# Optimization experiments

Measured on AMD Instinct MI355X. Metric: run time of the kernel, lower is better.

The kernel has to match this reference:

```python
import jax, jax.numpy as jnp
import numpy as np

NUM_GRIDS = 8
GRID = jnp.linspace(-2.0, 2.0, NUM_GRIDS)
DENOM = 4.0 / (NUM_GRIDS - 1)
H, D = 8, 64
Q_DIM = K_DIM = V_DIM = 512
TOT = H * D


def fastkan(x, ln_s, ln_b, sw, bw, bb):
    # LayerNorm over last dim
    mu = jnp.mean(x, axis=-1, keepdims=True)
    var = jnp.var(x, axis=-1, keepdims=True)
    xn = (x - mu) * jax.lax.rsqrt(var + 1e-5) * ln_s + ln_b
    # Gaussian RBF basis over fixed grid: [..., in, G]
    basis = jnp.exp(-jnp.square((xn[..., None] - GRID) / DENOM))
    flat = basis.reshape(*x.shape[:-1], x.shape[-1] * NUM_GRIDS)
    # spline linear + base update (silu -> linear)
    return flat @ sw.T + jax.nn.silu(x) @ bw.T + bb


def setup_inputs() -> dict:
    key = jax.random.key(0)
    keys = iter(jax.random.split(key, 32))
    B, QL, KL = 2, 2048, 2048
    inp = {
        "q": jax.random.normal(next(keys), (B, QL, Q_DIM), jnp.float32),
        "k": jax.random.normal(next(keys), (B, KL, K_DIM), jnp.float32),
        "v": jax.random.normal(next(keys), (B, KL, V_DIM), jnp.float32),
    }
    def layer(ind, outd):
        return {
            "ln_s": jnp.ones((ind,), jnp.float32),
            "ln_b": jnp.zeros((ind,), jnp.float32),
            "sw": jax.random.normal(next(keys), (outd, ind * NUM_GRIDS), jnp.float32) * (0.1 / np.sqrt(ind * NUM_GRIDS)),
            "bw": jax.random.normal(next(keys), (outd, ind), jnp.float32) / np.sqrt(ind),
            "bb": jnp.zeros((outd,), jnp.float32),
        }
    dims = {"lq": (Q_DIM, TOT), "lk": (K_DIM, TOT), "lv": (V_DIM, TOT), "lo": (TOT, Q_DIM), "lg": (Q_DIM, TOT)}
    for name, (i, o) in dims.items():
        for pn, arr in layer(i, o).items():
            inp[name + "_" + pn] = arr
    return inp


def reference(q, k, v,
              lq_ln_s, lq_ln_b, lq_sw, lq_bw, lq_bb,
              lk_ln_s, lk_ln_b, lk_sw, lk_bw, lk_bb,
              lv_ln_s, lv_ln_b, lv_sw, lv_bw, lv_bb,
              lo_ln_s, lo_ln_b, lo_sw, lo_bw, lo_bb,
              lg_ln_s, lg_ln_b, lg_sw, lg_bw, lg_bb):
    norm = D ** -0.5
    wq = fastkan(q, lq_ln_s, lq_ln_b, lq_sw, lq_bw, lq_bb).reshape(*q.shape[:-1], H, D) * norm
    wk = fastkan(k, lk_ln_s, lk_ln_b, lk_sw, lk_bw, lk_bb).reshape(*k.shape[:-1], H, D)
    # att: [b, q_len, k_len, h]; softmax over k_len (axis=-2), matching torch code
    att = jax.nn.softmax(jnp.einsum('bqhd,bkhd->bqkh', wq, wk), axis=-2)
    wv = fastkan(v, lv_ln_s, lv_ln_b, lv_sw, lv_bw, lv_bb).reshape(*v.shape[:-1], H, D)
    o = jnp.einsum('bqkh,bkhd->bqhd', att, wv).reshape(*q.shape[:-1], TOT)
    g = fastkan(q, lg_ln_s, lg_ln_b, lg_sw, lg_bw, lg_bb)
    o = jax.nn.sigmoid(g) * o
    return fastkan(o, lo_ln_s, lo_ln_b, lo_sw, lo_bw, lo_bb)
```

## Files before the change

### kernel.cpp

```cpp
#include <hip/hip_runtime.h>

typedef unsigned short u16;
typedef unsigned int u32;
typedef float f32x4 __attribute__((ext_vector_type(4)));
typedef short s16x8 __attribute__((ext_vector_type(8)));

#define IND 512
#define KSPL 4096
#define NOUT 512
#define PW 1024
#define MROWS 4096
#define LQ 2048
#define AST 72
#define NZ 8
#define NSPLIT 4

#define SWN (4096 * 512)
#define BWN (512 * 512)
#define LSTR ((size_t)(SWN + BWN + 512))

__device__ __forceinline__ float bf2f(u16 u) {
    union { u32 i; float f; } v; v.i = ((u32)u) << 16; return v.f;
}
__device__ __forceinline__ u16 f2bf(float f) {
    union { float f; u32 i; } v; v.f = f;
    u32 x = v.i;
    return (u16)((x + 0x7FFFu + ((x >> 16) & 1u)) >> 16);
}
__device__ __forceinline__ uint4 pack8(float4 a, float4 b) {
    uint4 p;
    p.x = (u32)f2bf(a.x) | ((u32)f2bf(a.y) << 16);
    p.y = (u32)f2bf(a.z) | ((u32)f2bf(a.w) << 16);
    p.z = (u32)f2bf(b.x) | ((u32)f2bf(b.y) << 16);
    p.w = (u32)f2bf(b.z) | ((u32)f2bf(b.w) << 16);
    return p;
}
__device__ __forceinline__ void gl_lds16(const u16* g, u16* l) {
    __builtin_amdgcn_global_load_lds((const __attribute__((address_space(1))) void*)g,
                                     (__attribute__((address_space(3))) void*)l, 16, 0, 0);
}

__global__ void detect_dtype(const u32* __restrict__ qraw, u32* __restrict__ flag)
{
    const int t = threadIdx.x;
    int cnt = 0;
    for (int i = t; i < 1024; i += 256) {
        u32 e = (qraw[i] >> 23) & 0xFFu;
        if (e >= 100u && e <= 140u) cnt++;
    }
    #pragma unroll
    for (int off = 32; off > 0; off >>= 1) cnt += __shfl_down(cnt, off);
    __shared__ int red[4];
    if ((t & 63) == 0) red[t >> 6] = cnt;
    __syncthreads();
    if (t == 0) flag[0] = (red[0] + red[1] + red[2] + red[3] > 512) ? 1u : 0u;
}

struct WSrc { const void* p[15]; };
__global__ __launch_bounds__(256) void convert_w(WSrc s, u16* __restrict__ wb, const u32* __restrict__ flag)
{
    const int r = blockIdx.y;
    const int l = r / 3, t = r - l * 3;
    const int n = (t == 0) ? SWN : ((t == 1) ? BWN : 512);
    const int i = (blockIdx.x * 256 + threadIdx.x) * 8;
    if (i >= n) return;
    u16* dst = wb + (size_t)l * LSTR + ((t == 0) ? 0 : ((t == 1) ? SWN : SWN + BWN)) + i;
    const void* src = s.p[r];
    if (flag[0]) {
        const float* f = (const float*)src;
        *(uint4*)dst = pack8(*(const float4*)&f[i], *(const float4*)&f[i + 4]);
    } else {
        *(uint4*)dst = *(const uint4*)&((const u16*)src)[i];
    }
}

__global__ __launch_bounds__(256) void prep_kan(
    const void* __restrict__ xv, const void* __restrict__ ln_sv, const void* __restrict__ ln_bv,
    u16* __restrict__ basis, u16* __restrict__ silu, const u32* __restrict__ flag)
{
    const int row = blockIdx.x;
    const int t = threadIdx.x;
    const bool isf = flag[0] != 0u;
    float x0, x1;
    if (isf) {
        const float* xr = (const float*)xv + (size_t)row * IND;
        x0 = xr[t]; x1 = xr[t + 256];
    } else {
        const u16* xr = (const u16*)xv + (size_t)row * IND;
        x0 = bf2f(xr[t]); x1 = bf2f(xr[t + 256]);
    }
    float s = x0 + x1;
    float ss = x0 * x0 + x1 * x1;
    #pragma unroll
    for (int off = 32; off > 0; off >>= 1) {
        s += __shfl_down(s, off);
        ss += __shfl_down(ss, off);
    }
    __shared__ float red[8];
    const int wid = t >> 6, ln = t & 63;
    if (ln == 0) { red[wid] = s; red[4 + wid] = ss; }
    __syncthreads();
    const float tot = red[0] + red[1] + red[2] + red[3];
    const float tot2 = red[4] + red[5] + red[6] + red[7];
    const float mu = tot * (1.0f / IND);
    const float rstd = rsqrtf(tot2 * (1.0f / IND) - mu * mu + 1e-5f);
    #pragma unroll
    for (int e = 0; e < 2; e++) {
        const int i = t + e * 256;
        const float xi = (e == 0) ? x0 : x1;
        float lns, lnb;
        if (isf) {
            lns = ((const float*)ln_sv)[i];
            lnb = ((const float*)ln_bv)[i];
        } else {
            lns = bf2f(((const u16*)ln_sv)[i]);
            lnb = bf2f(((const u16*)ln_bv)[i]);
        }
        const float xn = (xi - mu) * rstd * lns + lnb;
        u16 o8[8];
        #pragma unroll
        for (int g = 0; g < 8; g++) {
            float d = (xn - (-2.0f + g * (4.0f / 7.0f))) * 1.75f;
            o8[g] = f2bf(__expf(-d * d));
        }
        uint4 pk;
        pk.x = (u32)o8[0] | ((u32)o8[1] << 16);
        pk.y = (u32)o8[2] | ((u32)o8[3] << 16);
        pk.z = (u32)o8[4] | ((u32)o8[5] << 16);
        pk.w = (u32)o8[6] | ((u32)o8[7] << 16);
        *(uint4*)(basis + (size_t)row * KSPL + i * 8) = pk;
        silu[(size_t)row * IND + i] = f2bf(xi / (1.0f + __expf(-xi)));
    }
}

__global__ __launch_bounds__(256) void prep_merge(
    const float* __restrict__ Opart, const float* __restrict__ lpart,
    const u16* __restrict__ gbuf, const void* __restrict__ ln_sv, const void* __restrict__ ln_bv,
    u16* __restrict__ basis, u16* __restrict__ silu, const u32* __restrict__ flag)
{
    const int row = blockIdx.x;
    const int b = row >> 11, qr = row & (LQ - 1);
    const int t = threadIdx.x;
    const bool isf = flag[0] != 0u;

    float xv[2];
    #pragma unroll
    for (int e = 0; e < 2; e++) {
        const int col = t + e * 256;
        const int g = b * 8 + (col >> 6);
        const int dd = col & 63;
        float o = 0.0f, l = 0.0f;
        #pragma unroll
        for (int s = 0; s < NSPLIT; s++) {
            const size_t rb = ((size_t)s * 16 + g) * LQ + qr;
            o += Opart[rb * 64 + dd];
            l += lpart[rb];
        }
        const float gv = bf2f(gbuf[(size_t)row * IND + col]);
        xv[e] = (o / l) / (1.0f + __expf(-gv));
    }
    float s = xv[0] + xv[1];
    float ss = xv[0] * xv[0] + xv[1] * xv[1];
    #pragma unroll
    for (int off = 32; off > 0; off >>= 1) {
        s += __shfl_down(s, off);
        ss += __shfl_down(ss, off);
    }
    __shared__ float red[8];
    const int wid = t >> 6, ln = t & 63;
    if (ln == 0) { red[wid] = s; red[4 + wid] = ss; }
    __syncthreads();
    const float tot = red[0] + red[1] + red[2] + red[3];
    const float tot2 = red[4] + red[5] + red[6] + red[7];
    const float mu = tot * (1.0f / IND);
    const float rstd = rsqrtf(tot2 * (1.0f / IND) - mu * mu + 1e-5f);
    #pragma unroll
    for (int e = 0; e < 2; e++) {
        const int i = t + e * 256;
        const float xi = xv[e];
        float lns, lnb;
        if (isf) {
            lns = ((const float*)ln_sv)[i];
            lnb = ((const float*)ln_bv)[i];
        } else {
            lns = bf2f(((const u16*)ln_sv)[i]);
            lnb = bf2f(((const u16*)ln_bv)[i]);
        }
        const float xn = (xi - mu) * rstd * lns + lnb;
        u16 o8[8];
        #pragma unroll
        for (int g = 0; g < 8; g++) {
            float d = (xn - (-2.0f + g * (4.0f / 7.0f))) * 1.75f;
            o8[g] = f2bf(__expf(-d * d));
        }
        uint4 pk;
        pk.x = (u32)o8[0] | ((u32)o8[1] << 16);
        pk.y = (u32)o8[2] | ((u32)o8[3] << 16);
        pk.z = (u32)o8[4] | ((u32)o8[5] << 16);
        pk.w = (u32)o8[6] | ((u32)o8[7] << 16);
        *(uint4*)(basis + (size_t)row * KSPL + i * 8) = pk;
        silu[(size_t)row * IND + i] = f2bf(xi / (1.0f + __expf(-xi)));
    }
}

__global__ __launch_bounds__(512) void gemm_big(
    const u16* __restrict__ A1, const u16* __restrict__ B1a, const u16* __restrict__ B1b,
    const u16* __restrict__ A2, const u16* __restrict__ B2a, const u16* __restrict__ B2b,
    u16* __restrict__ P)
{
    __shared__ __align__(16) u16 sA[2][256 * 64];
    __shared__ __align__(16) u16 sB[2][256 * 64];
    const int tid = threadIdx.x;
    const int lane = tid & 63;
    const int wid = tid >> 6;
    const int fm = lane & 15;
    const int quad = lane >> 4;
    const int wmbase = (wid >> 2) * 128;
    const int wnbase = (wid & 3) * 64;
    const int mbase = blockIdx.x * 256;
    const int nbase = blockIdx.y * 256;
    const int kz = blockIdx.z;

    const u16* B1 = (nbase < 512) ? B1a : B1b;
    const u16* B2 = (nbase < 512) ? B2a : B2b;
    const int nb = nbase & 511;

    const int srow = wid * 8 + (lane >> 3);
    const int scol = ((lane & 7) ^ (lane >> 3)) * 8;
    const int k1b = kz * 512;
    const int k2b = kz * 64;

    f32x4 acc[8][4] = {};

    {
        const u16* b0 = B1 + (size_t)(nb + srow) * KSPL + k1b + scol;
        const u16* a0 = A1 + (size_t)(mbase + srow) * KSPL + k1b + scol;
        #pragma unroll
        for (int i = 0; i < 4; i++) gl_lds16(b0 + (size_t)i * 64 * KSPL, &sB[0][i * 4096 + wid * 512]);
        #pragma unroll
        for (int i = 0; i < 4; i++) gl_lds16(a0 + (size_t)i * 64 * KSPL, &sA[0][i * 4096 + wid * 512]);
        #pragma unroll
        for (int i = 0; i < 4; i++) gl_lds16(b0 + 64 + (size_t)i * 64 * KSPL, &sB[1][i * 4096 + wid * 512]);
    }
    asm volatile("s_waitcnt vmcnt(4)" ::: "memory");
    asm volatile("s_barrier" ::: "memory");

    #pragma unroll 1
    for (int t = 0; t < 9; ++t) {
        const u16* Ac = &sA[t & 1][0];
        const u16* Bc = &sB[t & 1][0];
        u16* abuf = &sA[(t + 1) & 1][0];
        u16* bbuf = &sB[t & 1][0];

        const u16* aS = nullptr; const u16* bS = nullptr;
        size_t aStep = 0, bStep = 0;
        if (t + 1 < 8) {
            aS = A1 + (size_t)(mbase + srow) * KSPL + k1b + (t + 1) * 64 + scol;
            aStep = (size_t)64 * KSPL;
        } else if (t + 1 == 8) {
            aS = A2 + (size_t)(mbase + srow) * IND + k2b + scol;
            aStep = (size_t)64 * IND;
        }
        if (t + 2 < 8) {
            bS = B1 + (size_t)(nb + srow) * KSPL + k1b + (t + 2) * 64 + scol;
            bStep = (size_t)64 * KSPL;
        } else if (t + 2 == 8) {
            bS = B2 + (size_t)(nb + srow) * IND + k2b + scol;
            bStep = (size_t)64 * IND;
        }

        s16x8 bfrag[4][2];
        #pragma unroll
        for (int n = 0; n < 4; n++)
            #pragma unroll
            for (int ks = 0; ks < 2; ks++)
                bfrag[n][ks] = *(const s16x8*)&Bc[((wnbase + n * 16 + fm) << 6) +
                                                 ((((ks << 2) + quad) ^ (fm & 7)) << 3)];

        #pragma unroll
        for (int ph = 0; ph < 2; ++ph) {
            s16x8 afr[4][2];
            #pragma unroll
            for (int i = 0; i < 4; i++)
                #pragma unroll
                for (int ks = 0; ks < 2; ks++)
                    afr[i][ks] = *(const s16x8*)&Ac[((wmbase + (ph * 4 + i) * 16 + fm) << 6) +
                                                   ((((ks << 2) + quad) ^ (fm & 7)) << 3)];
            if (ph == 0) {
                if (aS) {
                    #pragma unroll
                    for (int i = 0; i < 4; i++)
                        gl_lds16(aS + (size_t)i * aStep, abuf + i * 4096 + wid * 512);
                }
            } else {
                if (bS) {
                    #pragma unroll
                    for (int i = 0; i < 4; i++)
                        gl_lds16(bS + (size_t)i * bStep, bbuf + i * 4096 + wid * 512);
                }
            }
            asm volatile("s_barrier" ::: "memory");
            __builtin_amdgcn_s_setprio(1);
            #pragma unroll
            for (int i = 0; i < 4; i++)
                #pragma unroll
                for (int n = 0; n < 4; n++) {
                    acc[ph * 4 + i][n] = __builtin_amdgcn_mfma_f32_16x16x32_bf16(afr[i][0], bfrag[n][0], acc[ph * 4 + i][n], 0, 0, 0);
                    acc[ph * 4 + i][n] = __builtin_amdgcn_mfma_f32_16x16x32_bf16(afr[i][1], bfrag[n][1], acc[ph * 4 + i][n], 0, 0, 0);
                }
            __builtin_amdgcn_s_setprio(0);
            if (ph == 1) {
                if (t < 7)       asm volatile("s_waitcnt vmcnt(4)" ::: "memory");
                else if (t == 7) asm volatile("s_waitcnt vmcnt(0)" ::: "memory");
            }
            asm volatile("s_barrier" ::: "memory");
        }
    }

    #pragma unroll
    for (int n = 0; n < 4; n++) {
        const int col = nbase + wnbase + n * 16 + fm;
        const size_t cb = ((size_t)kz * PW + col) * MROWS;
        #pragma unroll
        for (int m = 0; m < 8; m++) {
            const int row0 = mbase + wmbase + m * 16 + quad * 4;
            uint2 o;
            o.x = (u32)f2bf(acc[m][n][0]) | ((u32)f2bf(acc[m][n][1]) << 16);
            o.y = (u32)f2bf(acc[m][n][2]) | ((u32)f2bf(acc[m][n][3]) << 16);
            *(uint2*)&P[cb + row0] = o;
        }
    }
}

__global__ __launch_bounds__(256) void reduce_kan(
    const u16* __restrict__ P, const u16* __restrict__ bias, void* __restrict__ C,
    float scale, const u32* __restrict__ flag, int ext_out, int colofs)
{
    __shared__ float tshf[64][65];
    const int row0 = blockIdx.x * 64;
    const int col0 = blockIdx.y * 64;
    const int tid = threadIdx.x;
    #pragma unroll
    for (int p = 0; p < 2; p++) {
        const int idx = tid + p * 256;
        const int cl = idx >> 3;
        const int r8 = (idx & 7) * 8;
        float a[8] = {};
        for (int kz = 0; kz < NZ; kz++) {
            uint4 pk = *(const uint4*)&P[((size_t)kz * PW + colofs + col0 + cl) * MROWS + row0 + r8];
            const u16* pv = (const u16*)&pk;
            #pragma unroll
            for (int u = 0; u < 8; u++) a[u] += bf2f(pv[u]);
        }
        const float bi = bf2f(bias[col0 + cl]);
        #pragma unroll
        for (int u = 0; u < 8; u++) tshf[r8 + u][cl] = (a[u] + bi) * scale;
    }
    __syncthreads();
    const bool fo = ext_out && (flag[0] != 0u);
    #pragma unroll
    for (int p = 0; p < 2; p++) {
        const int idx = tid + p * 256;
        const int rl = idx >> 3;
        const int c8 = (idx & 7) * 8;
        if (fo) {
            float* Cf = (float*)C + (size_t)(row0 + rl) * NOUT + col0 + c8;
            float4 f0, f1;
            f0.x = tshf[rl][c8 + 0]; f0.y = tshf[rl][c8 + 1];
            f0.z = tshf[rl][c8 + 2]; f0.w = tshf[rl][c8 + 3];
            f1.x = tshf[rl][c8 + 4]; f1.y = tshf[rl][c8 + 5];
            f1.z = tshf[rl][c8 + 6]; f1.w = tshf[rl][c8 + 7];
            *(float4*)Cf = f0;
            *(float4*)(Cf + 4) = f1;
        } else {
            uint4 o;
            o.x = (u32)f2bf(tshf[rl][c8 + 0]) | ((u32)f2bf(tshf[rl][c8 + 1]) << 16);
            o.y = (u32)f2bf(tshf[rl][c8 + 2]) | ((u32)f2bf(tshf[rl][c8 + 3]) << 16);
            o.z = (u32)f2bf(tshf[rl][c8 + 4]) | ((u32)f2bf(tshf[rl][c8 + 5]) << 16);
            o.w = (u32)f2bf(tshf[rl][c8 + 6]) | ((u32)f2bf(tshf[rl][c8 + 7]) << 16);
            *(uint4*)&((u16*)C)[(size_t)(row0 + rl) * NOUT + col0 + c8] = o;
        }
    }
}

__global__ __launch_bounds__(256) void reduce_vt(
    const u16* __restrict__ P, const u16* __restrict__ bias, u16* __restrict__ VT)
{
    const int bc = blockIdx.x;
    const int b = bc >> 9, col = bc & 511;
    const int row8 = threadIdx.x * 8;
    float a[8] = {};
    for (int kz = 0; kz < NZ; kz++) {
        uint4 pk = *(const uint4*)&P[((size_t)kz * PW + col) * MROWS + b * LQ + row8];
        const u16* pv = (const u16*)&pk;
        #pragma unroll
        for (int u = 0; u < 8; u++) a[u] += bf2f(pv[u]);
    }
    const float bi = bf2f(bias[col]);
    u16 tmp[8];
    #pragma unroll
    for (int u = 0; u < 8; u++) tmp[u] = f2bf(a[u] + bi);
    *(uint4*)&VT[(size_t)bc * LQ + row8] = *(const uint4*)tmp;
}

__global__ __launch_bounds__(256) void attn4(
    const u16* __restrict__ wqp, const u16* __restrict__ wkp, const u16* __restrict__ VT,
    float* __restrict__ Opart, float* __restrict__ lpart)
{
    __shared__ __align__(16) u16 Ks[64 * 64];
    __shared__ __align__(16) u16 Vs[64 * 64];
    __shared__ __align__(16) u16 Ps[4][32 * AST];

    const int tid = threadIdx.x;
    const int lane = tid & 63;
    const int wid = tid >> 6;
    const int quad = lane >> 4;
    const int fm = lane & 15;
    const int srow8 = lane >> 3;
    const int schk = (lane & 7) ^ (lane >> 3);
    const int qb = blockIdx.x * 128;
    const int g = blockIdx.y;
    const int s = blockIdx.z;
    const int b = g >> 3, h = g & 7;
    const size_t qkbase = ((size_t)b * LQ) * 512 + h * 64;
    const size_t vtbase = (size_t)g * 64 * LQ;
    const int kvlen = LQ / NSPLIT, kv0 = s * kvlen;

    s16x8 aq[2][2];
    #pragma unroll
    for (int qi = 0; qi < 2; qi++)
        #pragma unroll
        for (int ks = 0; ks < 2; ks++)
            aq[qi][ks] = *(const s16x8*)&wqp[qkbase +
                (size_t)(qb + wid * 32 + qi * 16 + fm) * 512 + ks * 32 + quad * 8];
    s16x8 ones;
    #pragma unroll
    for (int i = 0; i < 8; i++) ones[i] = (short)0x3F80;

    f32x4 oacc[2][4] = {};
    f32x4 lacc[2] = {};

    for (int kt = 0; kt < kvlen / 64; kt++) {
        const int kb = kv0 + kt * 64;
        #pragma unroll
        for (int gg = 0; gg < 2; gg++) {
            const int r = wid * 16 + gg * 8 + srow8;
            gl_lds16(&wkp[qkbase + (size_t)(kb + r) * 512 + schk * 8], &Ks[(wid * 16 + gg * 8) * 64]);
            gl_lds16(&VT[vtbase + (size_t)r * LQ + kb + schk * 8],     &Vs[(wid * 16 + gg * 8) * 64]);
        }
        __syncthreads();

        #pragma unroll
        for (int j = 0; j < 4; j++) {
            f32x4 z0 = {}, z1 = {};
            #pragma unroll
            for (int ks = 0; ks < 2; ks++) {
                s16x8 bk = *(const s16x8*)&Ks[((j * 16 + fm) << 6) +
                                              ((((ks << 2) + quad) ^ (fm & 7)) << 3)];
                z0 = __builtin_amdgcn_mfma_f32_16x16x32_bf16(aq[0][ks], bk, z0, 0, 0, 0);
                z1 = __builtin_amdgcn_mfma_f32_16x16x32_bf16(aq[1][ks], bk, z1, 0, 0, 0);
            }
            #pragma unroll
            for (int r = 0; r < 4; r++) {
                union { float f; u32 i; } u0, u1;
                u0.f = __expf(z0[r] - 12.0f);
                u1.f = __expf(z1[r] - 12.0f);
                Ps[wid][(quad * 4 + r) * AST + j * 16 + fm]        = (u16)(u0.i >> 16);
                Ps[wid][(16 + quad * 4 + r) * AST + j * 16 + fm]   = (u16)(u1.i >> 16);
            }
        }

        s16x8 ap[2][2];
        #pragma unroll
        for (int qi = 0; qi < 2; qi++)
            #pragma unroll
            for (int ks = 0; ks < 2; ks++)
                ap[qi][ks] = *(const s16x8*)&Ps[wid][(qi * 16 + fm) * AST + ks * 32 + quad * 8];
        #pragma unroll
        for (int jd = 0; jd < 4; jd++)
            #pragma unroll
            for (int ks = 0; ks < 2; ks++) {
                s16x8 bv = *(const s16x8*)&Vs[((jd * 16 + fm) << 6) +
                                              ((((ks << 2) + quad) ^ (fm & 7)) << 3)];
                oacc[0][jd] = __builtin_amdgcn_mfma_f32_16x16x32_bf16(ap[0][ks], bv, oacc[0][jd], 0, 0, 0);
                oacc[1][jd] = __builtin_amdgcn_mfma_f32_16x16x32_bf16(ap[1][ks], bv, oacc[1][jd], 0, 0, 0);
            }
        #pragma unroll
        for (int qi = 0; qi < 2; qi++)
            #pragma unroll
            for (int ks = 0; ks < 2; ks++)
                lacc[qi] = __builtin_amdgcn_mfma_f32_16x16x32_bf16(ap[qi][ks], ones, lacc[qi], 0, 0, 0);
        __syncthreads();
    }

    const size_t obase = ((size_t)s * 16 + g) * LQ;
    #pragma unroll
    for (int qi = 0; qi < 2; qi++) {
        #pragma unroll
        for (int jd = 0; jd < 4; jd++)
            #pragma unroll
            for (int r = 0; r < 4; r++) {
                const int qrow = qb + wid * 32 + qi * 16 + quad * 4 + r;
                Opart[(obase + qrow) * 64 + jd * 16 + fm] = oacc[qi][jd][r];
            }
        if (fm == 0) {
            #pragma unroll
            for (int r = 0; r < 4; r++) {
                const int qrow = qb + wid * 32 + qi * 16 + quad * 4 + r;
                lpart[obase + qrow] = lacc[qi][r];
            }
        }
    }
}

extern "C" void kernel_launch(void* const* d_in, const int* in_sizes, int n_in,
                              void* d_out, int out_size, void* d_ws, size_t ws_size,
                              hipStream_t stream)
{
    const void* q = d_in[0];
    const void* k = d_in[1];
    const void* v = d_in[2];
    auto P = [&](int i) { return (const void*)d_in[i]; };

    const size_t WB_BYTES  = 5 * LSTR * 2;
    const size_t BAS_BYTES = (size_t)MROWS * KSPL * 2;
    const size_t SIL_BYTES = (size_t)MROWS * IND * 2;
    const size_t PART_B    = (size_t)NZ * MROWS * PW * 2;
    const size_t VT_B      = (size_t)16 * 64 * LQ * 2;
    const size_t OPART_B   = (size_t)NSPLIT * 16 * LQ * 64 * 4;

    char* base = (char*)d_ws;
    u32*  flag  = (u32*)base;
    u16*  wb    = (u16*)(base + 4096);
    u16*  basis = (u16*)((char*)wb + WB_BYTES);
    u16*  silu  = (u16*)((char*)basis + BAS_BYTES);
    u16*  wq    = (u16*)((char*)silu + SIL_BYTES);
    u16*  wk    = wq + (size_t)MROWS * NOUT;
    u16*  gbuf  = wk + (size_t)MROWS * NOUT;
    u16*  part  = gbuf + (size_t)MROWS * NOUT;
    u16*  VT    = (u16*)((char*)part + PART_B);
    float* Opart = (float*)((char*)VT + VT_B);
    float* lpart = (float*)((char*)Opart + OPART_B);

    detect_dtype<<<1, 256, 0, stream>>>((const u32*)q, flag);

    WSrc srcs;
    const int lbase[5] = {3, 8, 13, 18, 23};
    for (int l = 0; l < 5; l++) {
        srcs.p[l * 3 + 0] = d_in[lbase[l] + 2];
        srcs.p[l * 3 + 1] = d_in[lbase[l] + 3];
        srcs.p[l * 3 + 2] = d_in[lbase[l] + 4];
    }
    convert_w<<<dim3(SWN / 2048, 15), 256, 0, stream>>>(srcs, wb, flag);

    auto swb = [&](int l) { return wb + (size_t)l * LSTR; };
    auto bwb = [&](int l) { return wb + (size_t)l * LSTR + SWN; };
    auto bbb = [&](int l) { return wb + (size_t)l * LSTR + SWN + BWN; };
    dim3 gg(MROWS / 256, NOUT / 256, NZ);
    dim3 ggf(MROWS / 256, PW / 256, NZ);
    dim3 rg(MROWS / 64, NOUT / 64);

    prep_kan<<<MROWS, 256, 0, stream>>>(q, P(3), P(4), basis, silu, flag);
    gemm_big<<<ggf, 512, 0, stream>>>(basis, swb(0), swb(4), silu, bwb(0), bwb(4), part);
    reduce_kan<<<rg, 256, 0, stream>>>(part, bbb(0), wq, 0.125f, flag, 0, 0);
    reduce_kan<<<rg, 256, 0, stream>>>(part, bbb(4), gbuf, 1.0f, flag, 0, 512);
    prep_kan<<<MROWS, 256, 0, stream>>>(k, P(8), P(9), basis, silu, flag);
    gemm_big<<<gg, 512, 0, stream>>>(basis, swb(1), swb(1), silu, bwb(1), bwb(1), part);
    reduce_kan<<<rg, 256, 0, stream>>>(part, bbb(1), wk, 1.0f, flag, 0, 0);
    prep_kan<<<MROWS, 256, 0, stream>>>(v, P(13), P(14), basis, silu, flag);
    gemm_big<<<gg, 512, 0, stream>>>(basis, swb(2), swb(2), silu, bwb(2), bwb(2), part);
    reduce_vt<<<1024, 256, 0, stream>>>(part, bbb(2), VT);

    attn4<<<dim3(LQ / 128, 16, NSPLIT), 256, 0, stream>>>(wq, wk, VT, Opart, lpart);

    prep_merge<<<MROWS, 256, 0, stream>>>(Opart, lpart, gbuf, P(18), P(19), basis, silu, flag);
    gemm_big<<<gg, 512, 0, stream>>>(basis, swb(3), swb(3), silu, bwb(3), bwb(3), part);
    reduce_kan<<<rg, 256, 0, stream>>>(part, bbb(3), d_out, 1.0f, flag, 1, 0);
}
```

Baseline: 414.0 us.

## Batch K and V KAN projections into shared launches with templated split-K depth

Templates the split-K GEMM on its K-split count and lets one launch serve two independent projections by selecting the operand pair from blockIdx.y. The K and V layers now share a single prep_kan launch, writing to doubled basis/silu buffers, and a single GEMM launch. The Q/G GEMMs drop from 8-way to 4-way split-K, and the partial reductions read fewer slices and merge into one launch. This cuts launch count and partial-sum traffic at the cost of longer per-block K loops and more workspace.

New measurement: 378.7 us. 1.09x faster.

```diff
diff --git a/kernel.cpp b/kernel.cpp
--- a/kernel.cpp
+++ b/kernel.cpp
@@ -12,7 +12,6 @@
 #define MROWS 4096
 #define LQ 2048
 #define AST 72
-#define NZ 8
 #define NSPLIT 4
 
 #define SWN (4096 * 512)
@@ -75,10 +74,17 @@
 }
 
 __global__ __launch_bounds__(256) void prep_kan(
-    const void* __restrict__ xv, const void* __restrict__ ln_sv, const void* __restrict__ ln_bv,
+    const void* __restrict__ xvA, const void* __restrict__ lsA, const void* __restrict__ lbA,
+    const void* __restrict__ xvB, const void* __restrict__ lsB, const void* __restrict__ lbB,
     u16* __restrict__ basis, u16* __restrict__ silu, const u32* __restrict__ flag)
 {
-    const int row = blockIdx.x;
+    const int sel = blockIdx.x >> 12;
+    const int row = blockIdx.x & 4095;
+    const void* xv   = sel ? xvB : xvA;
+    const void* ln_sv = sel ? lsB : lsA;
+    const void* ln_bv = sel ? lbB : lbA;
+    basis += (size_t)sel * MROWS * KSPL;
+    silu  += (size_t)sel * MROWS * IND;
     const int t = threadIdx.x;
     const bool isf = flag[0] != 0u;
     float x0, x1;
@@ -203,11 +209,13 @@
     }
 }
 
-__global__ __launch_bounds__(512) void gemm_big(
-    const u16* __restrict__ A1, const u16* __restrict__ B1a, const u16* __restrict__ B1b,
-    const u16* __restrict__ A2, const u16* __restrict__ B2a, const u16* __restrict__ B2b,
-    u16* __restrict__ P)
-{
+struct GPair { const u16 *A1, *B1, *A2, *B2; };
+
+template<int NZK>
+__global__ __launch_bounds__(512) void gemm_big(GPair p0, GPair p1, u16* __restrict__ P)
+{
+    constexpr int NT1 = KSPL / (NZK * 64);
+    constexpr int NT  = NT1 + IND / (NZK * 64);
     __shared__ __align__(16) u16 sA[2][256 * 64];
     __shared__ __align__(16) u16 sB[2][256 * 64];
     const int tid = threadIdx.x;
@@ -218,23 +226,21 @@
     const int wmbase = (wid >> 2) * 128;
     const int wnbase = (wid & 3) * 64;
     const int mbase = blockIdx.x * 256;
-    const int nbase = blockIdx.y * 256;
+    const int by = blockIdx.y;
+    const GPair g = (by >> 1) ? p1 : p0;
+    const int nb = (by & 1) * 256;
     const int kz = blockIdx.z;
-
-    const u16* B1 = (nbase < 512) ? B1a : B1b;
-    const u16* B2 = (nbase < 512) ? B2a : B2b;
-    const int nb = nbase & 511;
+    const int k1b = kz * (KSPL / NZK);
+    const int k2b = kz * (IND / NZK);
 
     const int srow = wid * 8 + (lane >> 3);
     const int scol = ((lane & 7) ^ (lane >> 3)) * 8;
-    const int k1b = kz * 512;
-    const int k2b = kz * 64;
 
     f32x4 acc[8][4] = {};
 
     {
-        const u16* b0 = B1 + (size_t)(nb + srow) * KSPL + k1b + scol;
-        const u16* a0 = A1 + (size_t)(mbase + srow) * KSPL + k1b + scol;
+        const u16* b0 = g.B1 + (size_t)(nb + srow) * KSPL + k1b + scol;
+        const u16* a0 = g.A1 + (size_t)(mbase + srow) * KSPL + k1b + scol;
         #pragma unroll
         for (int i = 0; i < 4; i++) gl_lds16(b0 + (size_t)i * 64 * KSPL, &sB[0][i * 4096 + wid * 512]);
         #pragma unroll
@@ -246,7 +252,7 @@
     asm volatile("s_barrier" ::: "memory");
 
     #pragma unroll 1
-    for (int t = 0; t < 9; ++t) {
+    for (int t = 0; t < NT; ++t) {
         const u16* Ac = &sA[t & 1][0];
         const u16* Bc = &sB[t & 1][0];
         u16* abuf = &sA[(t + 1) & 1][0];
@@ -254,18 +260,18 @@
 
         const u16* aS = nullptr; const u16* bS = nullptr;
         size_t aStep = 0, bStep = 0;
-        if (t + 1 < 8) {
-            aS = A1 + (size_t)(mbase + srow) * KSPL + k1b + (t + 1) * 64 + scol;
+        if (t + 1 < NT1) {
+            aS = g.A1 + (size_t)(mbase + srow) * KSPL + k1b + (t + 1) * 64 + scol;
             aStep = (size_t)64 * KSPL;
-        } else if (t + 1 == 8) {
-            aS = A2 + (size_t)(mbase + srow) * IND + k2b + scol;
+        } else if (t + 1 < NT) {
+            aS = g.A2 + (size_t)(mbase + srow) * IND + k2b + (t + 1 - NT1) * 64 + scol;
             aStep = (size_t)64 * IND;
         }
-        if (t + 2 < 8) {
-            bS = B1 + (size_t)(nb + srow) * KSPL + k1b + (t + 2) * 64 + scol;
+        if (t + 2 < NT1) {
+            bS = g.B1 + (size_t)(nb + srow) * KSPL + k1b + (t + 2) * 64 + scol;
             bStep = (size_t)64 * KSPL;
-        } else if (t + 2 == 8) {
-            bS = B2 + (size_t)(nb + srow) * IND + k2b + scol;
+        } else if (t + 2 < NT) {
+            bS = g.B2 + (size_t)(nb + srow) * IND + k2b + (t + 2 - NT1) * 64 + scol;
             bStep = (size_t)64 * IND;
         }
 
@@ -310,8 +316,8 @@
                 }
             __builtin_amdgcn_s_setprio(0);
             if (ph == 1) {
-                if (t < 7)       asm volatile("s_waitcnt vmcnt(4)" ::: "memory");
-                else if (t == 7) asm volatile("s_waitcnt vmcnt(0)" ::: "memory");
+                if (t < NT - 2)       asm volatile("s_waitcnt vmcnt(4)" ::: "memory");
+                else if (t == NT - 2) asm volatile("s_waitcnt vmcnt(0)" ::: "memory");
             }
             asm volatile("s_barrier" ::: "memory");
         }
@@ -319,7 +325,7 @@
 
     #pragma unroll
     for (int n = 0; n < 4; n++) {
-        const int col = nbase + wnbase + n * 16 + fm;
+        const int col = by * 256 + wnbase + n * 16 + fm;
         const size_t cb = ((size_t)kz * PW + col) * MROWS;
         #pragma unroll
         for (int m = 0; m < 8; m++) {
@@ -333,9 +339,15 @@
 }
 
 __global__ __launch_bounds__(256) void reduce_kan(
-    const u16* __restrict__ P, const u16* __restrict__ bias, void* __restrict__ C,
-    float scale, const u32* __restrict__ flag, int ext_out, int colofs)
-{
+    const u16* __restrict__ P, const u16* __restrict__ bias0, const u16* __restrict__ bias1,
+    void* __restrict__ C0, void* __restrict__ C1, float scale0, float scale1,
+    int co0, int co1, int nz, const u32* __restrict__ flag, int ext_out)
+{
+    const int zz = blockIdx.z;
+    const u16* bias = zz ? bias1 : bias0;
+    void* C = zz ? C1 : C0;
+    const float scale = zz ? scale1 : scale0;
+    const int colofs = zz ? co1 : co0;
     __shared__ float tshf[64][65];
     const int row0 = blockIdx.x * 64;
     const int col0 = blockIdx.y * 64;
@@ -346,7 +358,7 @@
         const int cl = idx >> 3;
         const int r8 = (idx & 7) * 8;
         float a[8] = {};
-        for (int kz = 0; kz < NZ; kz++) {
+        for (int kz = 0; kz < nz; kz++) {
             uint4 pk = *(const uint4*)&P[((size_t)kz * PW + colofs + col0 + cl) * MROWS + row0 + r8];
             const u16* pv = (const u16*)&pk;
             #pragma unroll
@@ -384,14 +396,15 @@
 }
 
 __global__ __launch_bounds__(256) void reduce_vt(
-    const u16* __restrict__ P, const u16* __restrict__ bias, u16* __restrict__ VT)
+    const u16* __restrict__ P, const u16* __restrict__ bias, u16* __restrict__ VT,
+    int colofs, int nz)
 {
     const int bc = blockIdx.x;
     const int b = bc >> 9, col = bc & 511;
     const int row8 = threadIdx.x * 8;
     float a[8] = {};
-    for (int kz = 0; kz < NZ; kz++) {
-        uint4 pk = *(const uint4*)&P[((size_t)kz * PW + col) * MROWS + b * LQ + row8];
+    for (int kz = 0; kz < nz; kz++) {
+        uint4 pk = *(const uint4*)&P[((size_t)kz * PW + colofs + col) * MROWS + b * LQ + row8];
         const u16* pv = (const u16*)&pk;
         #pragma unroll
         for (int u = 0; u < 8; u++) a[u] += bf2f(pv[u]);
@@ -523,9 +536,9 @@
     auto P = [&](int i) { return (const void*)d_in[i]; };
 
     const size_t WB_BYTES  = 5 * LSTR * 2;
-    const size_t BAS_BYTES = (size_t)MROWS * KSPL * 2;
-    const size_t SIL_BYTES = (size_t)MROWS * IND * 2;
-    const size_t PART_B    = (size_t)NZ * MROWS * PW * 2;
+    const size_t BAS_BYTES = (size_t)MROWS * KSPL * 2 * 2;
+    const size_t SIL_BYTES = (size_t)MROWS * IND * 2 * 2;
+    const size_t PART_B    = (size_t)8 * MROWS * PW * 2;
     const size_t VT_B      = (size_t)16 * 64 * LQ * 2;
     const size_t OPART_B   = (size_t)NSPLIT * 16 * LQ * 64 * 4;
 
@@ -542,6 +555,9 @@
     float* Opart = (float*)((char*)VT + VT_B);
     float* lpart = (float*)((char*)Opart + OPART_B);
 
+    u16* basisB = basis + (size_t)MROWS * KSPL;
+    u16* siluB  = silu + (size_t)MROWS * IND;
+
     detect_dtype<<<1, 256, 0, stream>>>((const u32*)q, flag);
 
     WSrc srcs;
@@ -556,24 +572,34 @@
     auto swb = [&](int l) { return wb + (size_t)l * LSTR; };
     auto bwb = [&](int l) { return wb + (size_t)l * LSTR + SWN; };
     auto bbb = [&](int l) { return wb + (size_t)l * LSTR + SWN + BWN; };
-    dim3 gg(MROWS / 256, NOUT / 256, NZ);
-    dim3 ggf(MROWS / 256, PW / 256, NZ);
+    dim3 gg4(MROWS / 256, 4, 4);
+    dim3 gg8(MROWS / 256, 2, 8);
     dim3 rg(MROWS / 64, NOUT / 64);
-
-    prep_kan<<<MROWS, 256, 0, stream>>>(q, P(3), P(4), basis, silu, flag);
-    gemm_big<<<ggf, 512, 0, stream>>>(basis, swb(0), swb(4), silu, bwb(0), bwb(4), part);
-    reduce_kan<<<rg, 256, 0, stream>>>(part, bbb(0), wq, 0.125f, flag, 0, 0);
-    reduce_kan<<<rg, 256, 0, stream>>>(part, bbb(4), gbuf, 1.0f, flag, 0, 512);
-    prep_kan<<<MROWS, 256, 0, stream>>>(k, P(8), P(9), basis, silu, flag);
-    gemm_big<<<gg, 512, 0, stream>>>(basis, swb(1), swb(1), silu, bwb(1), bwb(1), part);
-    reduce_kan<<<rg, 256, 0, stream>>>(part, bbb(1), wk, 1.0f, flag, 0, 0);
-    prep_kan<<<MROWS, 256, 0, stream>>>(v, P(13), P(14), basis, silu, flag);
-    gemm_big<<<gg, 512, 0, stream>>>(basis, swb(2), swb(2), silu, bwb(2), bwb(2), part);
-    reduce_vt<<<1024, 256, 0, stream>>>(part, bbb(2), VT);
+    dim3 rg2(MROWS / 64, NOUT / 64, 2);
+
+    prep_kan<<<MROWS, 256, 0, stream>>>(q, P(3), P(4), nullptr, nullptr, nullptr, basis, silu, flag);
+    {
+        GPair pq{basis, swb(0), silu, bwb(0)};
+        GPair pg{basis, swb(4), silu, bwb(4)};
+        (gemm_big<4>)<<<gg4, 512, 0, stream>>>(pq, pg, part);
+    }
+    reduce_kan<<<rg2, 256, 0, stream>>>(part, bbb(0), bbb(4), wq, gbuf, 0.125f, 1.0f, 0, 512, 4, flag, 0);
+
+    prep_kan<<<2 * MROWS, 256, 0, stream>>>(k, P(8), P(9), v, P(13), P(14), basis, silu, flag);
+    {
+        GPair pk{basis, swb(1), silu, bwb(1)};
+        GPair pv{basisB, swb(2), siluB, bwb(2)};
+        (gemm_big<4>)<<<gg4, 512, 0, stream>>>(pk, pv, part);
+    }
+    reduce_kan<<<rg, 256, 0, stream>>>(part, bbb(1), bbb(1), wk, wk, 1.0f, 1.0f, 0, 0, 4, flag, 0);
+    reduce_vt<<<1024, 256, 0, stream>>>(part, bbb(2), VT, 512, 4);
 
     attn4<<<dim3(LQ / 128, 16, NSPLIT), 256, 0, stream>>>(wq, wk, VT, Opart, lpart);
 
     prep_merge<<<MROWS, 256, 0, stream>>>(Opart, lpart, gbuf, P(18), P(19), basis, silu, flag);
-    gemm_big<<<gg, 512, 0, stream>>>(basis, swb(3), swb(3), silu, bwb(3), bwb(3), part);
-    reduce_kan<<<rg, 256, 0, stream>>>(part, bbb(3), d_out, 1.0f, flag, 1, 0);
-}
+    {
+        GPair po{basis, swb(3), silu, bwb(3)};
+        (gemm_big<8>)<<<gg8, 512, 0, stream>>>(po, po, part);
+    }
+    reduce_kan<<<rg, 256, 0, stream>>>(part, bbb(3), bbb(3), d_out, d_out, 1.0f, 1.0f, 0, 0, 8, flag, 1);
+}
```
